# Kernel tuning notes

Measured on AMD Instinct MI355X. Metric: run time of the kernel, lower is better.

The kernel has to match this reference:

```python
import jax, jax.numpy as jnp
import numpy as np

EPS = 1e-5

def _bn(x, gamma, beta):
    # training-mode BatchNorm1d over (batch, points) per channel; x: [B, C, N]
    mean = x.mean(axis=(0, 2), keepdims=True)
    var = x.var(axis=(0, 2), keepdims=True)
    return gamma[None, :, None] * (x - mean) * jax.lax.rsqrt(var + EPS) + beta[None, :, None]

def _conv_nn(x, idx, W, b):
    # x: [B, Cin, N_in]; idx: [N_out, k]; W: [Cout, Cin, k]
    g = x[:, :, idx]  # gather -> [B, Cin, N_out, k]
    return jnp.einsum('bink,oik->bon', g, W) + b[None, :, None]

def setup_inputs() -> dict:
    key = jax.random.key(0)
    ks = jax.random.split(key, 8)
    B, Cin, Cout = 32, 32, 64
    Nin, Nout, K, KP = 32768, 8192, 9, 4
    s = 0.05
    return {
        'x': jax.random.normal(ks[0], (B, Cin, Nin), jnp.float32),
        'W1': jax.random.normal(ks[1], (Cout, Cin, K), jnp.float32) * s,
        'b1': jnp.zeros((Cout,), jnp.float32),
        'W2': jax.random.normal(ks[2], (Cout, Cout, K), jnp.float32) * s,
        'b2': jnp.zeros((Cout,), jnp.float32),
        'We': jax.random.normal(ks[3], (Cout, Cin), jnp.float32) * s,
        'be': jnp.zeros((Cout,), jnp.float32),
        'g1': jnp.ones((Cout,), jnp.float32), 'beta1': jnp.zeros((Cout,), jnp.float32),
        'g2': jnp.ones((Cout,), jnp.float32), 'beta2': jnp.zeros((Cout,), jnp.float32),
        'g3': jnp.ones((Cout,), jnp.float32), 'beta3': jnp.zeros((Cout,), jnp.float32),
        'idx1': jax.random.randint(ks[4], (Nout, K), 0, Nin, jnp.int32),
        'idx2': jax.random.randint(ks[5], (Nout, K), 0, Nout, jnp.int32),
        'pool_idx': jax.random.randint(ks[6], (Nout, KP), 0, Nin, jnp.int32),
    }

def reference(x, W1, b1, W2, b2, We, be, g1, beta1, g2, beta2, g3, beta3, idx1, idx2, pool_idx):
    # main branch: ConvNN -> BN -> ReLU -> ConvNN -> BN
    out = jax.nn.relu(_bn(_conv_nn(x, idx1, W1, b1), g1, beta1))
    out = _bn(_conv_nn(out, idx2, W2, b2), g2, beta2)
    # shortcut: AvgPoolNN (k=4) -> 1x1 conv expand -> BN
    pooled = x[:, :, pool_idx].mean(axis=-1)  # [B, Cin, N_out]
    identity = _bn(jnp.einsum('bin,oi->bon', pooled, We) + be[None, :, None], g3, beta3)
    return jax.nn.relu(out + identity)
```

## Files before the change

kernel.cpp:

```cpp
#include <hip/hip_runtime.h>

typedef __attribute__((ext_vector_type(8))) short short8_t;
typedef __attribute__((ext_vector_type(4))) float f32x4_t;

#define NOUT 8192
#define NIN 32768
#define MTOT 262144.0f
#define ST_STRIPES 64

static __device__ __forceinline__ float bf2f(ushort u) {
    union { float f; unsigned int i; } x; x.i = ((unsigned int)u) << 16; return x.f;
}
static __device__ __forceinline__ ushort f2bf(float f) {
    union { float f; unsigned int i; } x; x.f = f;
    unsigned int r = x.i + 0x7fffu + ((x.i >> 16) & 1u);
    return (ushort)(r >> 16);
}

static __device__ __forceinline__ int4 bnx(int4 v, const float* __restrict__ acs, int ch0) {
    ushort* pv = (ushort*)&v;
    #pragma unroll
    for (int e = 0; e < 8; ++e) {
        float f = acs[ch0 + e] * bf2f(pv[e]) + acs[64 + ch0 + e];
        pv[e] = f2bf(fmaxf(f, 0.f));
    }
    return v;
}

__global__ __launch_bounds__(256) void transpose_x_kernel(
    const float* __restrict__ x, ushort* __restrict__ xt)
{
    __shared__ ushort T[64][66];
    const int tid = threadIdx.x;
    const int n0 = blockIdx.x * 64, c0 = blockIdx.y * 64;
    const int lane64 = tid & 63, rb = (tid >> 6) * 16;
    #pragma unroll
    for (int r = 0; r < 16; ++r) {
        int c_l = rb + r;
        T[c_l][lane64] = f2bf(x[(size_t)(c0 + c_l) * NIN + n0 + lane64]);
    }
    __syncthreads();
    #pragma unroll
    for (int r = 0; r < 16; ++r) {
        int n_l = rb + r;
        xt[(size_t)(n0 + n_l) * 1024 + c0 + lane64] = T[lane64][n_l];
    }
}

__global__ __launch_bounds__(256) void prep_w_kernel(
    const float* __restrict__ W1, const float* __restrict__ W2,
    const float* __restrict__ We,
    ushort* __restrict__ w1p, ushort* __restrict__ w2p, ushort* __restrict__ wep,
    float* __restrict__ stz)
{
    int t = blockIdx.x * 256 + threadIdx.x;
    const int N1 = 9 * 64 * 32, N2 = 9 * 64 * 64, N3 = 64 * 32;
    if (t < 3 * ST_STRIPES * 128) stz[t] = 0.f;
    if (t < N1) {
        int k = t >> 11, rem = t & 2047, o = rem >> 5, i = rem & 31;
        w1p[t] = f2bf(W1[o * 288 + i * 9 + k]);
    } else if (t < N1 + N2) {
        int t2 = t - N1;
        int k = t2 >> 12, rem = t2 & 4095, o = rem >> 6, ci = rem & 63;
        w2p[t2] = f2bf(W2[o * 576 + ci * 9 + k]);
    } else if (t < N1 + N2 + N3) {
        int t3 = t - N1 - N2;
        wep[t3] = f2bf(We[t3]);
    }
}

__global__ __launch_bounds__(256) void conv1_kernel(
    const ushort* __restrict__ xt, const int* __restrict__ idx1,
    const ushort* __restrict__ w1p, ushort* __restrict__ out1,
    float* __restrict__ st)
{
    __shared__ ushort As[128 * 40];
    __shared__ ushort Ws[64 * 40];
    __shared__ float Ls[128];
    const int tid = threadIdx.x;
    const int lane = tid & 63, wv = tid >> 6;
    const int nbase = blockIdx.x * 4;
    const int r_st = tid >> 1, h_st = tid & 1;
    const int nl_st = tid >> 6, b_st = r_st & 31;
    const int o_st = tid >> 2, sg_st = tid & 3;

    f32x4_t acc[2][4];
    #pragma unroll
    for (int m = 0; m < 2; ++m)
        #pragma unroll
        for (int nt = 0; nt < 4; ++nt) acc[m][nt] = (f32x4_t){0.f, 0.f, 0.f, 0.f};

    {
        int rrow = idx1[(nbase + nl_st) * 9];
        const int4* src = (const int4*)(xt + (size_t)rrow * 1024 + b_st * 32 + h_st * 16);
        int4* dst = (int4*)(As + r_st * 40 + h_st * 16);
        dst[0] = src[0]; dst[1] = src[1];
        const int4* wsrc = (const int4*)(w1p + o_st * 32 + sg_st * 8);
        *(int4*)(Ws + o_st * 40 + sg_st * 8) = wsrc[0];
    }
    if (tid < 128) Ls[tid] = 0.f;
    __syncthreads();

    for (int k = 0; k < 9; ++k) {
        int4 pa0, pa1, pw;
        const bool pre = (k + 1 < 9);
        if (pre) {
            int rrow = idx1[(nbase + nl_st) * 9 + k + 1];
            const int4* src = (const int4*)(xt + (size_t)rrow * 1024 + b_st * 32 + h_st * 16);
            pa0 = src[0]; pa1 = src[1];
            pw = *(const int4*)(w1p + (k + 1) * 2048 + o_st * 32 + sg_st * 8);
        }
        short8_t af[2], bfr[4];
        #pragma unroll
        for (int m = 0; m < 2; ++m)
            af[m] = *(const short8_t*)(As + (wv * 32 + m * 16 + (lane & 15)) * 40 + (lane >> 4) * 8);
        #pragma unroll
        for (int nt = 0; nt < 4; ++nt)
            bfr[nt] = *(const short8_t*)(Ws + (nt * 16 + (lane & 15)) * 40 + (lane >> 4) * 8);
        #pragma unroll
        for (int m = 0; m < 2; ++m)
            #pragma unroll
            for (int nt = 0; nt < 4; ++nt)
                acc[m][nt] = __builtin_amdgcn_mfma_f32_16x16x32_bf16(af[m], bfr[nt], acc[m][nt], 0, 0, 0);
        __syncthreads();
        if (pre) {
            int4* dst = (int4*)(As + r_st * 40 + h_st * 16);
            dst[0] = pa0; dst[1] = pa1;
            *(int4*)(Ws + o_st * 40 + sg_st * 8) = pw;
        }
        __syncthreads();
    }

    #pragma unroll
    for (int m = 0; m < 2; ++m)
        #pragma unroll
        for (int nt = 0; nt < 4; ++nt)
            #pragma unroll
            for (int j = 0; j < 4; ++j) {
                int row = wv * 32 + m * 16 + (lane >> 4) * 4 + j;
                int nl = row >> 5, bb = row & 31, col = nt * 16 + (lane & 15);
                out1[(size_t)(nbase + nl) * 2048 + bb * 64 + col] = f2bf(acc[m][nt][j]);
            }
    #pragma unroll
    for (int nt = 0; nt < 4; ++nt) {
        float s = 0.f, q = 0.f;
        #pragma unroll
        for (int m = 0; m < 2; ++m)
            #pragma unroll
            for (int j = 0; j < 4; ++j) { float v = acc[m][nt][j]; s += v; q += v * v; }
        s += __shfl_xor(s, 16); s += __shfl_xor(s, 32);
        q += __shfl_xor(q, 16); q += __shfl_xor(q, 32);
        if (lane < 16) {
            atomicAdd(&Ls[nt * 16 + lane], s);
            atomicAdd(&Ls[64 + nt * 16 + lane], q);
        }
    }
    __syncthreads();
    if (tid < 128) atomicAdd(&st[(blockIdx.x & (ST_STRIPES - 1)) * 128 + tid], Ls[tid]);
}

__global__ __launch_bounds__(256) void conv2_kernel(
    const ushort* __restrict__ out1raw, const int* __restrict__ idx2,
    const ushort* __restrict__ w2p, const float* __restrict__ ac1,
    ushort* __restrict__ out2, float* __restrict__ st)
{
    __shared__ ushort As[128 * 72];
    __shared__ ushort Ws[64 * 72];
    __shared__ float Ls[128];
    __shared__ float ACs[128];
    const int tid = threadIdx.x;
    const int lane = tid & 63, wv = tid >> 6;
    const int nbase = blockIdx.x * 4;
    const int r_st = tid >> 1, h_st = tid & 1;
    const int nl_st = tid >> 6, b_st = r_st & 31;
    const int o_st = tid >> 2, sg_st = tid & 3;
    const int ch0 = h_st * 32;

    f32x4_t acc[2][4];
    #pragma unroll
    for (int m = 0; m < 2; ++m)
        #pragma unroll
        for (int nt = 0; nt < 4; ++nt) acc[m][nt] = (f32x4_t){0.f, 0.f, 0.f, 0.f};

    if (tid < 128) { ACs[tid] = ac1[tid]; Ls[tid] = 0.f; }

    int4 q0, q1, q2, q3;
    {
        int rrow = idx2[(nbase + nl_st) * 9];
        const int4* src = (const int4*)(out1raw + (size_t)rrow * 2048 + b_st * 64 + h_st * 32);
        q0 = src[0]; q1 = src[1]; q2 = src[2]; q3 = src[3];
        const int4* wsrc = (const int4*)(w2p + o_st * 64 + sg_st * 16);
        int4* wdst = (int4*)(Ws + o_st * 72 + sg_st * 16);
        wdst[0] = wsrc[0]; wdst[1] = wsrc[1];
    }
    __syncthreads();
    {
        int4* dst = (int4*)(As + r_st * 72 + h_st * 32);
        dst[0] = bnx(q0, ACs, ch0);
        dst[1] = bnx(q1, ACs, ch0 + 8);
        dst[2] = bnx(q2, ACs, ch0 + 16);
        dst[3] = bnx(q3, ACs, ch0 + 24);
    }
    __syncthreads();

    for (int k = 0; k < 9; ++k) {
        int4 pa0, pa1, pa2, pa3, pw0, pw1;
        const bool pre = (k + 1 < 9);
        if (pre) {
            int rrow = idx2[(nbase + nl_st) * 9 + k + 1];
            const int4* src = (const int4*)(out1raw + (size_t)rrow * 2048 + b_st * 64 + h_st * 32);
            pa0 = src[0]; pa1 = src[1]; pa2 = src[2]; pa3 = src[3];
            const int4* wsrc = (const int4*)(w2p + (k + 1) * 4096 + o_st * 64 + sg_st * 16);
            pw0 = wsrc[0]; pw1 = wsrc[1];
        }
        #pragma unroll
        for (int kk = 0; kk < 2; ++kk) {
            short8_t af[2], bfr[4];
            #pragma unroll
            for (int m = 0; m < 2; ++m)
                af[m] = *(const short8_t*)(As + (wv * 32 + m * 16 + (lane & 15)) * 72 + kk * 32 + (lane >> 4) * 8);
            #pragma unroll
            for (int nt = 0; nt < 4; ++nt)
                bfr[nt] = *(const short8_t*)(Ws + (nt * 16 + (lane & 15)) * 72 + kk * 32 + (lane >> 4) * 8);
            #pragma unroll
            for (int m = 0; m < 2; ++m)
                #pragma unroll
                for (int nt = 0; nt < 4; ++nt)
                    acc[m][nt] = __builtin_amdgcn_mfma_f32_16x16x32_bf16(af[m], bfr[nt], acc[m][nt], 0, 0, 0);
        }
        if (pre) {
            pa0 = bnx(pa0, ACs, ch0);
            pa1 = bnx(pa1, ACs, ch0 + 8);
            pa2 = bnx(pa2, ACs, ch0 + 16);
            pa3 = bnx(pa3, ACs, ch0 + 24);
        }
        __syncthreads();
        if (pre) {
            int4* dst = (int4*)(As + r_st * 72 + h_st * 32);
            dst[0] = pa0; dst[1] = pa1; dst[2] = pa2; dst[3] = pa3;
            int4* wdst = (int4*)(Ws + o_st * 72 + sg_st * 16);
            wdst[0] = pw0; wdst[1] = pw1;
        }
        __syncthreads();
    }

    #pragma unroll
    for (int m = 0; m < 2; ++m)
        #pragma unroll
        for (int nt = 0; nt < 4; ++nt)
            #pragma unroll
            for (int j = 0; j < 4; ++j) {
                int row = wv * 32 + m * 16 + (lane >> 4) * 4 + j;
                int nl = row >> 5, bb = row & 31, col = nt * 16 + (lane & 15);
                out2[(size_t)(nbase + nl) * 2048 + bb * 64 + col] = f2bf(acc[m][nt][j]);
            }
    #pragma unroll
    for (int nt = 0; nt < 4; ++nt) {
        float s = 0.f, q = 0.f;
        #pragma unroll
        for (int m = 0; m < 2; ++m)
            #pragma unroll
            for (int j = 0; j < 4; ++j) { float v = acc[m][nt][j]; s += v; q += v * v; }
        s += __shfl_xor(s, 16); s += __shfl_xor(s, 32);
        q += __shfl_xor(q, 16); q += __shfl_xor(q, 32);
        if (lane < 16) {
            atomicAdd(&Ls[nt * 16 + lane], s);
            atomicAdd(&Ls[64 + nt * 16 + lane], q);
        }
    }
    __syncthreads();
    if (tid < 128) atomicAdd(&st[(blockIdx.x & (ST_STRIPES - 1)) * 128 + tid], Ls[tid]);
}

__global__ __launch_bounds__(256) void ident_kernel(
    const ushort* __restrict__ xt, const int* __restrict__ pool_idx,
    const ushort* __restrict__ wep, ushort* __restrict__ identt,
    float* __restrict__ st)
{
    __shared__ ushort As[256 * 40];
    __shared__ ushort Ws[64 * 40];
    __shared__ float Ls[128];
    const int tid = threadIdx.x;
    const int lane = tid & 63, wv = tid >> 6;
    const int nbase = blockIdx.x * 8;
    const int n_l = tid >> 5, b = tid & 31;

    float pa[32];
    #pragma unroll
    for (int i = 0; i < 32; ++i) pa[i] = 0.f;
    for (int kp = 0; kp < 4; ++kp) {
        int rrow = pool_idx[(nbase + n_l) * 4 + kp];
        const int4* src = (const int4*)(xt + (size_t)rrow * 1024 + b * 32);
        #pragma unroll
        for (int j = 0; j < 4; ++j) {
            int4 v = src[j];
            const ushort* pv = (const ushort*)&v;
            #pragma unroll
            for (int e = 0; e < 8; ++e) pa[j * 8 + e] += bf2f(pv[e]);
        }
    }
    {
        int4* dst = (int4*)(As + (n_l * 32 + b) * 40);
        #pragma unroll
        for (int j = 0; j < 4; ++j) {
            int4 v; ushort* pv = (ushort*)&v;
            #pragma unroll
            for (int e = 0; e < 8; ++e) pv[e] = f2bf(pa[j * 8 + e] * 0.25f);
            dst[j] = v;
        }
    }
    {
        int o = tid >> 2, seg = tid & 3;
        *(int4*)(Ws + o * 40 + seg * 8) = *(const int4*)(wep + o * 32 + seg * 8);
    }
    if (tid < 128) Ls[tid] = 0.f;
    __syncthreads();

    f32x4_t acc[4][4];
    #pragma unroll
    for (int m = 0; m < 4; ++m)
        #pragma unroll
        for (int nt = 0; nt < 4; ++nt) acc[m][nt] = (f32x4_t){0.f, 0.f, 0.f, 0.f};
    short8_t af[4], bfr[4];
    #pragma unroll
    for (int m = 0; m < 4; ++m)
        af[m] = *(const short8_t*)(As + (wv * 64 + m * 16 + (lane & 15)) * 40 + (lane >> 4) * 8);
    #pragma unroll
    for (int nt = 0; nt < 4; ++nt)
        bfr[nt] = *(const short8_t*)(Ws + (nt * 16 + (lane & 15)) * 40 + (lane >> 4) * 8);
    #pragma unroll
    for (int m = 0; m < 4; ++m)
        #pragma unroll
        for (int nt = 0; nt < 4; ++nt)
            acc[m][nt] = __builtin_amdgcn_mfma_f32_16x16x32_bf16(af[m], bfr[nt], acc[m][nt], 0, 0, 0);

    #pragma unroll
    for (int m = 0; m < 4; ++m)
        #pragma unroll
        for (int nt = 0; nt < 4; ++nt)
            #pragma unroll
            for (int j = 0; j < 4; ++j) {
                int row = wv * 64 + m * 16 + (lane >> 4) * 4 + j;
                int nl = row >> 5, bb = row & 31, col = nt * 16 + (lane & 15);
                identt[(size_t)(nbase + nl) * 2048 + bb * 64 + col] = f2bf(acc[m][nt][j]);
            }
    #pragma unroll
    for (int nt = 0; nt < 4; ++nt) {
        float s = 0.f, q = 0.f;
        #pragma unroll
        for (int m = 0; m < 4; ++m)
            #pragma unroll
            for (int j = 0; j < 4; ++j) { float v = acc[m][nt][j]; s += v; q += v * v; }
        s += __shfl_xor(s, 16); s += __shfl_xor(s, 32);
        q += __shfl_xor(q, 16); q += __shfl_xor(q, 32);
        if (lane < 16) {
            atomicAdd(&Ls[nt * 16 + lane], s);
            atomicAdd(&Ls[64 + nt * 16 + lane], q);
        }
    }
    __syncthreads();
    if (tid < 128) atomicAdd(&st[(blockIdx.x & (ST_STRIPES - 1)) * 128 + tid], Ls[tid]);
}

__global__ void finalize_kernel(const float* __restrict__ st, const float* __restrict__ g,
                                const float* __restrict__ bet, float* __restrict__ ac)
{
    int o = threadIdx.x;
    if (o >= 64) return;
    float s = 0.f, q = 0.f;
    for (int i = 0; i < ST_STRIPES; ++i) { s += st[i * 128 + o]; q += st[i * 128 + 64 + o]; }
    float mean = s * (1.0f / MTOT);
    float var  = q * (1.0f / MTOT) - mean * mean;
    float a = g[o] * rsqrtf(var + 1e-5f);
    ac[o] = a;
    ac[64 + o] = bet[o] - a * mean;
}

__global__ void finalize23_kernel(
    const float* __restrict__ st2, const float* __restrict__ g2, const float* __restrict__ b2,
    const float* __restrict__ st3, const float* __restrict__ g3, const float* __restrict__ b3,
    float* __restrict__ ac2, float* __restrict__ ac3)
{
    int o = threadIdx.x;
    if (o >= 64) return;
    const float* st = blockIdx.x ? st3 : st2;
    const float* g  = blockIdx.x ? g3  : g2;
    const float* bt = blockIdx.x ? b3  : b2;
    float* ac       = blockIdx.x ? ac3 : ac2;
    float s = 0.f, q = 0.f;
    for (int i = 0; i < ST_STRIPES; ++i) { s += st[i * 128 + o]; q += st[i * 128 + 64 + o]; }
    float mean = s * (1.0f / MTOT);
    float var  = q * (1.0f / MTOT) - mean * mean;
    float a = g[o] * rsqrtf(var + 1e-5f);
    ac[o] = a;
    ac[64 + o] = bt[o] - a * mean;
}

__global__ __launch_bounds__(256) void final_combine_kernel(
    const ushort* __restrict__ out2, const ushort* __restrict__ idt,
    const float* __restrict__ ac2, const float* __restrict__ ac3,
    float* __restrict__ dout)
{
    __shared__ float tile[64][65];
    const int tid = threadIdx.x;
    const int n0 = blockIdx.x * 64, bo0 = blockIdx.y * 64;
    const int lane64 = tid & 63, rb = (tid >> 6) * 16;
    const int o = lane64;
    const float a2 = ac2[o], c2 = ac2[64 + o], a3 = ac3[o], c3 = ac3[64 + o];
    #pragma unroll
    for (int r = 0; r < 16; ++r) {
        int n_l = rb + r;
        size_t p = (size_t)(n0 + n_l) * 2048 + bo0 + lane64;
        float v = a2 * bf2f(out2[p]) + c2 + a3 * bf2f(idt[p]) + c3;
        tile[n_l][lane64] = fmaxf(v, 0.f);
    }
    __syncthreads();
    #pragma unroll
    for (int r = 0; r < 16; ++r) {
        int bo_l = rb + r;
        dout[(size_t)(bo0 + bo_l) * NOUT + n0 + lane64] = tile[lane64][bo_l];
    }
}

extern "C" void kernel_launch(void* const* d_in, const int* in_sizes, int n_in,
                              void* d_out, int out_size, void* d_ws, size_t ws_size,
                              hipStream_t stream)
{
    const float* x     = (const float*)d_in[0];
    const float* W1    = (const float*)d_in[1];
    const float* W2    = (const float*)d_in[3];
    const float* We    = (const float*)d_in[5];
    const float* g1    = (const float*)d_in[7];
    const float* beta1 = (const float*)d_in[8];
    const float* g2    = (const float*)d_in[9];
    const float* beta2 = (const float*)d_in[10];
    const float* g3    = (const float*)d_in[11];
    const float* beta3 = (const float*)d_in[12];
    const int* idx1    = (const int*)d_in[13];
    const int* idx2    = (const int*)d_in[14];
    const int* pool_idx= (const int*)d_in[15];
    float* dout = (float*)d_out;

    char* ws = (char*)d_ws;
    const size_t off_xt   = 0;
    const size_t off_out1 = 67108864;
    const size_t off_out2 = 100663296;
    const size_t off_id   = 134217728;
    const size_t off_w1p  = 167772160;
    const size_t off_w2p  = 167809024;
    const size_t off_wep  = 167882752;
    const size_t off_st   = 167886848;
    const size_t off_ac   = 167985152;
    const size_t need     = 167986688;
    if (ws_size < need) return;

    ushort* xt   = (ushort*)(ws + off_xt);
    ushort* out1 = (ushort*)(ws + off_out1);
    ushort* out2 = (ushort*)(ws + off_out2);
    ushort* idt  = (ushort*)(ws + off_id);
    ushort* w1p  = (ushort*)(ws + off_w1p);
    ushort* w2p  = (ushort*)(ws + off_w2p);
    ushort* wep  = (ushort*)(ws + off_wep);
    float*  st1  = (float*)(ws + off_st);
    float*  st2  = st1 + 64 * 128;
    float*  st3  = st1 + 2 * 64 * 128;
    float*  ac1  = (float*)(ws + off_ac);
    float*  ac2  = ac1 + 128;
    float*  ac3  = ac1 + 256;

    prep_w_kernel<<<224, 256, 0, stream>>>(W1, W2, We, w1p, w2p, wep, st1);
    transpose_x_kernel<<<dim3(512, 16), 256, 0, stream>>>(x, xt);
    conv1_kernel<<<2048, 256, 0, stream>>>(xt, idx1, w1p, out1, st1);
    ident_kernel<<<1024, 256, 0, stream>>>(xt, pool_idx, wep, idt, st3);
    finalize_kernel<<<1, 64, 0, stream>>>(st1, g1, beta1, ac1);
    conv2_kernel<<<2048, 256, 0, stream>>>(out1, idx2, w2p, ac1, out2, st2);
    finalize23_kernel<<<2, 64, 0, stream>>>(st2, g2, beta2, st3, g3, beta3, ac2, ac3);
    final_combine_kernel<<<dim3(128, 32), 256, 0, stream>>>(out2, idt, ac2, ac3, dout);
}
```

Before: 191.0 us.

## Give each wavefront its own output point and drop block-wide barriers in conv kernels

Conv1 and conv2 now give each wavefront one output point with private double-buffered LDS tiles, so the per-tap __syncthreads pairs are gone. Weight fragments are read straight from global memory (L1/L2) instead of being staged in shared memory. The ident kernel also reads weights directly. The BN scale and shift used in conv2 are kept in registers per lane. The hand-written bf16 rounding is replaced by the HIP intrinsic. The risk is more global weight traffic per wave, and correctness now depends on intra-wave LDS ordering enforced only by compiler barriers.

After: 219.1 us. +14.7%, slower.

```diff
diff --git a/kernel.cpp b/kernel.cpp
--- a/kernel.cpp
+++ b/kernel.cpp
@@ -1,4 +1,5 @@
 #include <hip/hip_runtime.h>
+#include <hip/hip_bf16.h>
 
 typedef __attribute__((ext_vector_type(8))) short short8_t;
 typedef __attribute__((ext_vector_type(4))) float f32x4_t;
@@ -8,22 +9,22 @@
 #define MTOT 262144.0f
 #define ST_STRIPES 64
 
+#define MF(a,b,c) __builtin_amdgcn_mfma_f32_16x16x32_bf16((a),(b),(c),0,0,0)
+
 static __device__ __forceinline__ float bf2f(ushort u) {
     union { float f; unsigned int i; } x; x.i = ((unsigned int)u) << 16; return x.f;
 }
-static __device__ __forceinline__ ushort f2bf(float f) {
-    union { float f; unsigned int i; } x; x.f = f;
-    unsigned int r = x.i + 0x7fffu + ((x.i >> 16) & 1u);
-    return (ushort)(r >> 16);
-}
-
-static __device__ __forceinline__ int4 bnx(int4 v, const float* __restrict__ acs, int ch0) {
+static __device__ __forceinline__ ushort f2bfx(float f) {
+    union { __hip_bfloat16 h; ushort u; } v;
+    v.h = __float2bfloat16(f);
+    return v.u;
+}
+
+static __device__ __forceinline__ int4 bn8(int4 v, const float* a8, const float* c8) {
     ushort* pv = (ushort*)&v;
     #pragma unroll
-    for (int e = 0; e < 8; ++e) {
-        float f = acs[ch0 + e] * bf2f(pv[e]) + acs[64 + ch0 + e];
-        pv[e] = f2bf(fmaxf(f, 0.f));
-    }
+    for (int e = 0; e < 8; ++e)
+        pv[e] = f2bfx(fmaxf(a8[e] * bf2f(pv[e]) + c8[e], 0.f));
     return v;
 }
 
@@ -37,7 +38,7 @@
     #pragma unroll
     for (int r = 0; r < 16; ++r) {
         int c_l = rb + r;
-        T[c_l][lane64] = f2bf(x[(size_t)(c0 + c_l) * NIN + n0 + lane64]);
+        T[c_l][lane64] = f2bfx(x[(size_t)(c0 + c_l) * NIN + n0 + lane64]);
     }
     __syncthreads();
     #pragma unroll
@@ -58,14 +59,14 @@
     if (t < 3 * ST_STRIPES * 128) stz[t] = 0.f;
     if (t < N1) {
         int k = t >> 11, rem = t & 2047, o = rem >> 5, i = rem & 31;
-        w1p[t] = f2bf(W1[o * 288 + i * 9 + k]);
+        w1p[t] = f2bfx(W1[o * 288 + i * 9 + k]);
     } else if (t < N1 + N2) {
         int t2 = t - N1;
         int k = t2 >> 12, rem = t2 & 4095, o = rem >> 6, ci = rem & 63;
-        w2p[t2] = f2bf(W2[o * 576 + ci * 9 + k]);
+        w2p[t2] = f2bfx(W2[o * 576 + ci * 9 + k]);
     } else if (t < N1 + N2 + N3) {
         int t3 = t - N1 - N2;
-        wep[t3] = f2bf(We[t3]);
+        wep[t3] = f2bfx(We[t3]);
     }
 }
 
@@ -74,15 +75,20 @@
     const ushort* __restrict__ w1p, ushort* __restrict__ out1,
     float* __restrict__ st)
 {
-    __shared__ ushort As[128 * 40];
-    __shared__ ushort Ws[64 * 40];
+    __shared__ __align__(16) ushort As[4 * 2 * 32 * 40];
     __shared__ float Ls[128];
     const int tid = threadIdx.x;
     const int lane = tid & 63, wv = tid >> 6;
-    const int nbase = blockIdx.x * 4;
-    const int r_st = tid >> 1, h_st = tid & 1;
-    const int nl_st = tid >> 6, b_st = r_st & 31;
-    const int o_st = tid >> 2, sg_st = tid & 3;
+    const int n = __builtin_amdgcn_readfirstlane(blockIdx.x * 4 + wv);
+    const int bb = lane >> 1, hf = lane & 1;
+    const int fr = (lane & 15) * 40, fc = (lane >> 4) * 8;
+    ushort* Ab0 = As + wv * (2 * 32 * 40);
+    ushort* Ab1 = Ab0 + 32 * 40;
+    const int* idxn = idx1 + n * 9;
+    const ushort* wbase = w1p + (lane & 15) * 32 + fc;
+
+    if (tid < 128) Ls[tid] = 0.f;
+    __syncthreads();
 
     f32x4_t acc[2][4];
     #pragma unroll
@@ -90,56 +96,50 @@
         #pragma unroll
         for (int nt = 0; nt < 4; ++nt) acc[m][nt] = (f32x4_t){0.f, 0.f, 0.f, 0.f};
 
-    {
-        int rrow = idx1[(nbase + nl_st) * 9];
-        const int4* src = (const int4*)(xt + (size_t)rrow * 1024 + b_st * 32 + h_st * 16);
-        int4* dst = (int4*)(As + r_st * 40 + h_st * 16);
-        dst[0] = src[0]; dst[1] = src[1];
-        const int4* wsrc = (const int4*)(w1p + o_st * 32 + sg_st * 8);
-        *(int4*)(Ws + o_st * 40 + sg_st * 8) = wsrc[0];
-    }
-    if (tid < 128) Ls[tid] = 0.f;
-    __syncthreads();
-
-    for (int k = 0; k < 9; ++k) {
-        int4 pa0, pa1, pw;
-        const bool pre = (k + 1 < 9);
-        if (pre) {
-            int rrow = idx1[(nbase + nl_st) * 9 + k + 1];
-            const int4* src = (const int4*)(xt + (size_t)rrow * 1024 + b_st * 32 + h_st * 16);
-            pa0 = src[0]; pa1 = src[1];
-            pw = *(const int4*)(w1p + (k + 1) * 2048 + o_st * 32 + sg_st * 8);
-        }
-        short8_t af[2], bfr[4];
-        #pragma unroll
-        for (int m = 0; m < 2; ++m)
-            af[m] = *(const short8_t*)(As + (wv * 32 + m * 16 + (lane & 15)) * 40 + (lane >> 4) * 8);
+    int4 A0[2], A1[2];
+
+#define C1_LOAD(K, A) { \
+    const ushort* rp = xt + (size_t)idxn[K] * 1024 + bb * 32 + hf * 16; \
+    A[0] = *(const int4*)rp; A[1] = *(const int4*)(rp + 8); }
+
+#define C1_BODY(K, A, ab) { \
+    const ushort* wp = wbase + (K) * 2048; \
+    short8_t b0 = *(const short8_t*)(wp); \
+    short8_t b1 = *(const short8_t*)(wp + 512); \
+    short8_t b2 = *(const short8_t*)(wp + 1024); \
+    short8_t b3 = *(const short8_t*)(wp + 1536); \
+    ushort* wr = (ab) + bb * 40 + hf * 16; \
+    *(int4*)wr = A[0]; *(int4*)(wr + 8) = A[1]; \
+    asm volatile("" ::: "memory"); \
+    short8_t af0 = *(const short8_t*)((ab) + fr + fc); \
+    short8_t af1 = *(const short8_t*)((ab) + fr + 640 + fc); \
+    asm volatile("" ::: "memory"); \
+    acc[0][0] = MF(af0, b0, acc[0][0]); acc[1][0] = MF(af1, b0, acc[1][0]); \
+    acc[0][1] = MF(af0, b1, acc[0][1]); acc[1][1] = MF(af1, b1, acc[1][1]); \
+    acc[0][2] = MF(af0, b2, acc[0][2]); acc[1][2] = MF(af1, b2, acc[1][2]); \
+    acc[0][3] = MF(af0, b3, acc[0][3]); acc[1][3] = MF(af1, b3, acc[1][3]); }
+
+    C1_LOAD(0, A0);
+    for (int t = 0; t < 4; ++t) {
+        C1_LOAD(2 * t + 1, A1);
+        C1_BODY(2 * t, A0, Ab0);
+        C1_LOAD(2 * t + 2, A0);
+        C1_BODY(2 * t + 1, A1, Ab1);
+    }
+    C1_BODY(8, A0, Ab0);
+#undef C1_LOAD
+#undef C1_BODY
+
+    const size_t outbase = (size_t)n * 2048;
+    #pragma unroll
+    for (int m = 0; m < 2; ++m)
         #pragma unroll
         for (int nt = 0; nt < 4; ++nt)
-            bfr[nt] = *(const short8_t*)(Ws + (nt * 16 + (lane & 15)) * 40 + (lane >> 4) * 8);
-        #pragma unroll
-        for (int m = 0; m < 2; ++m)
-            #pragma unroll
-            for (int nt = 0; nt < 4; ++nt)
-                acc[m][nt] = __builtin_amdgcn_mfma_f32_16x16x32_bf16(af[m], bfr[nt], acc[m][nt], 0, 0, 0);
-        __syncthreads();
-        if (pre) {
-            int4* dst = (int4*)(As + r_st * 40 + h_st * 16);
-            dst[0] = pa0; dst[1] = pa1;
-            *(int4*)(Ws + o_st * 40 + sg_st * 8) = pw;
-        }
-        __syncthreads();
-    }
-
-    #pragma unroll
-    for (int m = 0; m < 2; ++m)
-        #pragma unroll
-        for (int nt = 0; nt < 4; ++nt)
             #pragma unroll
             for (int j = 0; j < 4; ++j) {
-                int row = wv * 32 + m * 16 + (lane >> 4) * 4 + j;
-                int nl = row >> 5, bb = row & 31, col = nt * 16 + (lane & 15);
-                out1[(size_t)(nbase + nl) * 2048 + bb * 64 + col] = f2bf(acc[m][nt][j]);
+                int b = m * 16 + (lane >> 4) * 4 + j;
+                int o = nt * 16 + (lane & 15);
+                out1[outbase + b * 64 + o] = f2bfx(acc[m][nt][j]);
             }
     #pragma unroll
     for (int nt = 0; nt < 4; ++nt) {
@@ -164,17 +164,31 @@
     const ushort* __restrict__ w2p, const float* __restrict__ ac1,
     ushort* __restrict__ out2, float* __restrict__ st)
 {
-    __shared__ ushort As[128 * 72];
-    __shared__ ushort Ws[64 * 72];
+    __shared__ __align__(16) ushort As[4 * 2 * 32 * 72];
     __shared__ float Ls[128];
-    __shared__ float ACs[128];
     const int tid = threadIdx.x;
     const int lane = tid & 63, wv = tid >> 6;
-    const int nbase = blockIdx.x * 4;
-    const int r_st = tid >> 1, h_st = tid & 1;
-    const int nl_st = tid >> 6, b_st = r_st & 31;
-    const int o_st = tid >> 2, sg_st = tid & 3;
-    const int ch0 = h_st * 32;
+    const int n = __builtin_amdgcn_readfirstlane(blockIdx.x * 4 + wv);
+    const int chg = lane & 7, bq = lane >> 3;
+    const int fr = (lane & 15) * 72, fc = (lane >> 4) * 8;
+    ushort* Ab0 = As + wv * (2 * 32 * 72);
+    ushort* Ab1 = Ab0 + 32 * 72;
+    const int* idxn = idx2 + n * 9;
+    const ushort* wbase = w2p + (lane & 15) * 64 + fc;
+
+    float a8[8], c8[8];
+    {
+        const float4 av0 = *(const float4*)(ac1 + chg * 8);
+        const float4 av1 = *(const float4*)(ac1 + chg * 8 + 4);
+        const float4 cv0 = *(const float4*)(ac1 + 64 + chg * 8);
+        const float4 cv1 = *(const float4*)(ac1 + 64 + chg * 8 + 4);
+        a8[0]=av0.x; a8[1]=av0.y; a8[2]=av0.z; a8[3]=av0.w;
+        a8[4]=av1.x; a8[5]=av1.y; a8[6]=av1.z; a8[7]=av1.w;
+        c8[0]=cv0.x; c8[1]=cv0.y; c8[2]=cv0.z; c8[3]=cv0.w;
+        c8[4]=cv1.x; c8[5]=cv1.y; c8[6]=cv1.z; c8[7]=cv1.w;
+    }
+    if (tid < 128) Ls[tid] = 0.f;
+    __syncthreads();
 
     f32x4_t acc[2][4];
     #pragma unroll
@@ -182,77 +196,60 @@
         #pragma unroll
         for (int nt = 0; nt < 4; ++nt) acc[m][nt] = (f32x4_t){0.f, 0.f, 0.f, 0.f};
 
-    if (tid < 128) { ACs[tid] = ac1[tid]; Ls[tid] = 0.f; }
-
-    int4 q0, q1, q2, q3;
-    {
-        int rrow = idx2[(nbase + nl_st) * 9];
-        const int4* src = (const int4*)(out1raw + (size_t)rrow * 2048 + b_st * 64 + h_st * 32);
-        q0 = src[0]; q1 = src[1]; q2 = src[2]; q3 = src[3];
-        const int4* wsrc = (const int4*)(w2p + o_st * 64 + sg_st * 16);
-        int4* wdst = (int4*)(Ws + o_st * 72 + sg_st * 16);
-        wdst[0] = wsrc[0]; wdst[1] = wsrc[1];
-    }
-    __syncthreads();
-    {
-        int4* dst = (int4*)(As + r_st * 72 + h_st * 32);
-        dst[0] = bnx(q0, ACs, ch0);
-        dst[1] = bnx(q1, ACs, ch0 + 8);
-        dst[2] = bnx(q2, ACs, ch0 + 16);
-        dst[3] = bnx(q3, ACs, ch0 + 24);
-    }
-    __syncthreads();
-
-    for (int k = 0; k < 9; ++k) {
-        int4 pa0, pa1, pa2, pa3, pw0, pw1;
-        const bool pre = (k + 1 < 9);
-        if (pre) {
-            int rrow = idx2[(nbase + nl_st) * 9 + k + 1];
-            const int4* src = (const int4*)(out1raw + (size_t)rrow * 2048 + b_st * 64 + h_st * 32);
-            pa0 = src[0]; pa1 = src[1]; pa2 = src[2]; pa3 = src[3];
-            const int4* wsrc = (const int4*)(w2p + (k + 1) * 4096 + o_st * 64 + sg_st * 16);
-            pw0 = wsrc[0]; pw1 = wsrc[1];
-        }
-        #pragma unroll
-        for (int kk = 0; kk < 2; ++kk) {
-            short8_t af[2], bfr[4];
-            #pragma unroll
-            for (int m = 0; m < 2; ++m)
-                af[m] = *(const short8_t*)(As + (wv * 32 + m * 16 + (lane & 15)) * 72 + kk * 32 + (lane >> 4) * 8);
-            #pragma unroll
-            for (int nt = 0; nt < 4; ++nt)
-                bfr[nt] = *(const short8_t*)(Ws + (nt * 16 + (lane & 15)) * 72 + kk * 32 + (lane >> 4) * 8);
-            #pragma unroll
-            for (int m = 0; m < 2; ++m)
-                #pragma unroll
-                for (int nt = 0; nt < 4; ++nt)
-                    acc[m][nt] = __builtin_amdgcn_mfma_f32_16x16x32_bf16(af[m], bfr[nt], acc[m][nt], 0, 0, 0);
-        }
-        if (pre) {
-            pa0 = bnx(pa0, ACs, ch0);
-            pa1 = bnx(pa1, ACs, ch0 + 8);
-            pa2 = bnx(pa2, ACs, ch0 + 16);
-            pa3 = bnx(pa3, ACs, ch0 + 24);
-        }
-        __syncthreads();
-        if (pre) {
-            int4* dst = (int4*)(As + r_st * 72 + h_st * 32);
-            dst[0] = pa0; dst[1] = pa1; dst[2] = pa2; dst[3] = pa3;
-            int4* wdst = (int4*)(Ws + o_st * 72 + sg_st * 16);
-            wdst[0] = pw0; wdst[1] = pw1;
-        }
-        __syncthreads();
-    }
-
+    int4 A0[4], A1[4];
+
+#define C2_LOAD(K, A) { \
+    const ushort* rp = out1raw + (size_t)idxn[K] * 2048 + bq * 256 + chg * 8; \
+    A[0] = *(const int4*)rp;         A[1] = *(const int4*)(rp + 64); \
+    A[2] = *(const int4*)(rp + 128); A[3] = *(const int4*)(rp + 192); }
+
+#define C2_BODY(K, A, ab) { \
+    const ushort* wp = wbase + (K) * 4096; \
+    short8_t b0 = *(const short8_t*)(wp);        short8_t b1 = *(const short8_t*)(wp + 32); \
+    short8_t b2 = *(const short8_t*)(wp + 1024); short8_t b3 = *(const short8_t*)(wp + 1056); \
+    short8_t b4 = *(const short8_t*)(wp + 2048); short8_t b5 = *(const short8_t*)(wp + 2080); \
+    short8_t b6 = *(const short8_t*)(wp + 3072); short8_t b7 = *(const short8_t*)(wp + 3104); \
+    int4 t0 = bn8(A[0], a8, c8), t1 = bn8(A[1], a8, c8); \
+    int4 t2 = bn8(A[2], a8, c8), t3 = bn8(A[3], a8, c8); \
+    ushort* wr = (ab) + bq * 288 + chg * 8; \
+    *(int4*)(wr) = t0; *(int4*)(wr + 72) = t1; \
+    *(int4*)(wr + 144) = t2; *(int4*)(wr + 216) = t3; \
+    asm volatile("" ::: "memory"); \
+    short8_t af00 = *(const short8_t*)((ab) + fr + fc); \
+    short8_t af01 = *(const short8_t*)((ab) + fr + 32 + fc); \
+    short8_t af10 = *(const short8_t*)((ab) + fr + 1152 + fc); \
+    short8_t af11 = *(const short8_t*)((ab) + fr + 1184 + fc); \
+    asm volatile("" ::: "memory"); \
+    acc[0][0] = MF(af00, b0, acc[0][0]); acc[0][0] = MF(af01, b1, acc[0][0]); \
+    acc[0][1] = MF(af00, b2, acc[0][1]); acc[0][1] = MF(af01, b3, acc[0][1]); \
+    acc[0][2] = MF(af00, b4, acc[0][2]); acc[0][2] = MF(af01, b5, acc[0][2]); \
+    acc[0][3] = MF(af00, b6, acc[0][3]); acc[0][3] = MF(af01, b7, acc[0][3]); \
+    acc[1][0] = MF(af10, b0, acc[1][0]); acc[1][0] = MF(af11, b1, acc[1][0]); \
+    acc[1][1] = MF(af10, b2, acc[1][1]); acc[1][1] = MF(af11, b3, acc[1][1]); \
+    acc[1][2] = MF(af10, b4, acc[1][2]); acc[1][2] = MF(af11, b5, acc[1][2]); \
+    acc[1][3] = MF(af10, b6, acc[1][3]); acc[1][3] = MF(af11, b7, acc[1][3]); }
+
+    C2_LOAD(0, A0);
+    for (int t = 0; t < 4; ++t) {
+        C2_LOAD(2 * t + 1, A1);
+        C2_BODY(2 * t, A0, Ab0);
+        C2_LOAD(2 * t + 2, A0);
+        C2_BODY(2 * t + 1, A1, Ab1);
+    }
+    C2_BODY(8, A0, Ab0);
+#undef C2_LOAD
+#undef C2_BODY
+
+    const size_t outbase = (size_t)n * 2048;
     #pragma unroll
     for (int m = 0; m < 2; ++m)
         #pragma unroll
         for (int nt = 0; nt < 4; ++nt)
             #pragma unroll
             for (int j = 0; j < 4; ++j) {
-                int row = wv * 32 + m * 16 + (lane >> 4) * 4 + j;
-                int nl = row >> 5, bb = row & 31, col = nt * 16 + (lane & 15);
-                out2[(size_t)(nbase + nl) * 2048 + bb * 64 + col] = f2bf(acc[m][nt][j]);
+                int b = m * 16 + (lane >> 4) * 4 + j;
+                int o = nt * 16 + (lane & 15);
+                out2[outbase + b * 64 + o] = f2bfx(acc[m][nt][j]);
             }
     #pragma unroll
     for (int nt = 0; nt < 4; ++nt) {
@@ -277,14 +274,16 @@
     const ushort* __restrict__ wep, ushort* __restrict__ identt,
     float* __restrict__ st)
 {
-    __shared__ ushort As[256 * 40];
-    __shared__ ushort Ws[64 * 40];
+    __shared__ __align__(16) ushort As[256 * 40];
     __shared__ float Ls[128];
     const int tid = threadIdx.x;
     const int lane = tid & 63, wv = tid >> 6;
     const int nbase = blockIdx.x * 8;
     const int n_l = tid >> 5, b = tid & 31;
 
+    if (tid < 128) Ls[tid] = 0.f;
+    __syncthreads();
+
     float pa[32];
     #pragma unroll
     for (int i = 0; i < 32; ++i) pa[i] = 0.f;
@@ -305,34 +304,31 @@
         for (int j = 0; j < 4; ++j) {
             int4 v; ushort* pv = (ushort*)&v;
             #pragma unroll
-            for (int e = 0; e < 8; ++e) pv[e] = f2bf(pa[j * 8 + e] * 0.25f);
+            for (int e = 0; e < 8; ++e) pv[e] = f2bfx(pa[j * 8 + e] * 0.25f);
             dst[j] = v;
         }
     }
-    {
-        int o = tid >> 2, seg = tid & 3;
-        *(int4*)(Ws + o * 40 + seg * 8) = *(const int4*)(wep + o * 32 + seg * 8);
-    }
-    if (tid < 128) Ls[tid] = 0.f;
-    __syncthreads();
-
-    f32x4_t acc[4][4];
-    #pragma unroll
-    for (int m = 0; m < 4; ++m)
-        #pragma unroll
-        for (int nt = 0; nt < 4; ++nt) acc[m][nt] = (f32x4_t){0.f, 0.f, 0.f, 0.f};
+    asm volatile("" ::: "memory");
+
     short8_t af[4], bfr[4];
     #pragma unroll
     for (int m = 0; m < 4; ++m)
         af[m] = *(const short8_t*)(As + (wv * 64 + m * 16 + (lane & 15)) * 40 + (lane >> 4) * 8);
+    const ushort* wpf = wep + (lane & 15) * 32 + (lane >> 4) * 8;
     #pragma unroll
     for (int nt = 0; nt < 4; ++nt)
-        bfr[nt] = *(const short8_t*)(Ws + (nt * 16 + (lane & 15)) * 40 + (lane >> 4) * 8);
+        bfr[nt] = *(const short8_t*)(wpf + nt * 512);
+
+    f32x4_t acc[4][4];
     #pragma unroll
     for (int m = 0; m < 4; ++m)
         #pragma unroll
+        for (int nt = 0; nt < 4; ++nt) acc[m][nt] = (f32x4_t){0.f, 0.f, 0.f, 0.f};
+    #pragma unroll
+    for (int m = 0; m < 4; ++m)
+        #pragma unroll
         for (int nt = 0; nt < 4; ++nt)
-            acc[m][nt] = __builtin_amdgcn_mfma_f32_16x16x32_bf16(af[m], bfr[nt], acc[m][nt], 0, 0, 0);
+            acc[m][nt] = MF(af[m], bfr[nt], acc[m][nt]);
 
     #pragma unroll
     for (int m = 0; m < 4; ++m)
@@ -342,7 +338,7 @@
             for (int j = 0; j < 4; ++j) {
                 int row = wv * 64 + m * 16 + (lane >> 4) * 4 + j;
                 int nl = row >> 5, bb = row & 31, col = nt * 16 + (lane & 15);
-                identt[(size_t)(nbase + nl) * 2048 + bb * 64 + col] = f2bf(acc[m][nt][j]);
+                identt[(size_t)(nbase + nl) * 2048 + bb * 64 + col] = f2bfx(acc[m][nt][j]);
             }
     #pragma unroll
     for (int nt = 0; nt < 4; ++nt) {
```
